# Kernel optimization log

Measured on AMD Instinct MI355X. Metric: run time of the kernel, lower is better.

The kernel has to match this reference:

```python
import jax, jax.numpy as jnp
import numpy as np

N_NODES = 100000


def _gcn_conv(x, W, b, src, dst, num_nodes):
    """PyG-style GCNConv: add self-loops, symmetric normalization, linear.
    x: [N, Fin], W: [Fin, Fout], b: [Fout], src/dst: [E] (already include self-loops).
    """
    h = x @ W  # [N, Fout] transform first (PyG order), keeps edge traffic at Fout width
    ones = jnp.ones(dst.shape[0], dtype=h.dtype)
    deg = jax.ops.segment_sum(ones, dst, num_segments=num_nodes)  # degree of A+I
    dinv = jnp.where(deg > 0, jax.lax.rsqrt(deg), 0.0)
    norm = dinv[src] * dinv[dst]  # [E]
    msg = h[src] * norm[:, None]  # [E, Fout] gather + scale
    out = jax.ops.segment_sum(msg, dst, num_segments=num_nodes)  # scatter-add
    return out + b


def setup_inputs() -> dict:
    key = jax.random.key(0)
    k1, k2, k3, k4, k5 = jax.random.split(key, 5)
    input_dim, hidden_dim, embedding_dim = 128, 64, 32
    x = jax.random.normal(k1, (N_NODES, input_dim), dtype=jnp.float32)
    edge_index = jax.random.randint(k2, (2, 1600000), 0, N_NODES, dtype=jnp.int32)
    # Glorot-like init for weights
    W1 = jax.random.normal(k3, (input_dim, hidden_dim), dtype=jnp.float32) / np.sqrt(input_dim)
    b1 = jnp.zeros((hidden_dim,), dtype=jnp.float32)
    W2 = jax.random.normal(k4, (hidden_dim, embedding_dim), dtype=jnp.float32) / np.sqrt(hidden_dim)
    b2 = jnp.zeros((embedding_dim,), dtype=jnp.float32)
    return {"x": x, "edge_index": edge_index, "W1": W1, "b1": b1, "W2": W2, "b2": b2}


def reference(x, edge_index, W1, b1, W2, b2):
    num_nodes = x.shape[0]
    loop = jnp.arange(num_nodes, dtype=edge_index.dtype)
    src = jnp.concatenate([edge_index[0], loop])  # add self-loops (PyG default)
    dst = jnp.concatenate([edge_index[1], loop])
    h = _gcn_conv(x, W1, b1, src, dst, num_nodes)
    h = jax.nn.relu(h)
    z = _gcn_conv(h, W2, b2, src, dst, num_nodes)
    return z
```

## Files before the change

kernel.cpp:

```cpp
#include <hip/hip_runtime.h>
#include <hip/hip_bf16.h>


#define MAXBUCK 512
#define CURSTRIDE 16

typedef unsigned int uint32;

__device__ __forceinline__ void fma4(float4& a, float s, const float4& w) {
    a.x = fmaf(s, w.x, a.x); a.y = fmaf(s, w.y, a.y);
    a.z = fmaf(s, w.z, a.z); a.w = fmaf(s, w.w, a.w);
}
__device__ __forceinline__ uint32 bf16rn(float f) {
    uint32 u = __float_as_uint(f);
    return (u + 0x7fffu + ((u >> 16) & 1u)) >> 16;
}
__device__ __forceinline__ float bflo(uint32 v) { return __uint_as_float(v << 16); }
__device__ __forceinline__ float bfhi(uint32 v) { return __uint_as_float(v & 0xffff0000u); }

__global__ __launch_bounds__(1024) void k_bin(const int* __restrict__ src,
                                              const int* __restrict__ dst, int E,
                                              int nbuck, int cap,
                                              int* __restrict__ cursor,
                                              uint32* __restrict__ pairs) {
    __shared__ int hist[MAXBUCK];
    __shared__ int base_l[MAXBUCK];
    __shared__ int cur[MAXBUCK];
    __shared__ int dloc[4096];
    int t = threadIdx.x;
    int e0 = blockIdx.x * 4096;
    for (int i = t; i < MAXBUCK; i += 1024) { hist[i] = 0; cur[i] = 0; }
    __syncthreads();
    for (int i = t; i < 4096; i += 1024) {
        int e = e0 + i;
        if (e < E) {
            int d = dst[e];
            dloc[i] = d;
            atomicAdd(&hist[d >> 8], 1);
        }
    }
    __syncthreads();
    for (int i = t; i < nbuck; i += 1024)
        base_l[i] = hist[i] ? (i * cap + atomicAdd(&cursor[i * CURSTRIDE], hist[i])) : 0;
    __syncthreads();
    for (int i = t; i < 4096; i += 1024) {
        int e = e0 + i;
        if (e < E) {
            int d = dloc[i];
            int b = d >> 8;
            int p = atomicAdd(&cur[b], 1);
            int idx = base_l[b] + p;
            if (idx < (b + 1) * cap)
                pairs[idx] = (uint32)src[e] | ((uint32)(d & 255) << 24);
        }
    }
}

__global__ __launch_bounds__(1024) void k_fill2(const uint32* __restrict__ pairs,
                                                const int* __restrict__ bucket_cnt,
                                                int cap, int N,
                                                int* __restrict__ srclist,
                                                int* __restrict__ rowstart,
                                                int* __restrict__ cnt,
                                                float* __restrict__ dinv) {
    __shared__ int hist[256];
    __shared__ int sh[256];
    __shared__ int rs_ex[256];
    __shared__ int cur[256];
    int b = blockIdx.x;
    int t = threadIdx.x;
    int start = b * cap;
    int end = start + min(bucket_cnt[b * CURSTRIDE], cap);
    int node0 = b << 8;

    if (t < 256) { hist[t] = 0; cur[t] = 0; }
    __syncthreads();
    for (int e = start + t; e < end; e += 1024)
        atomicAdd(&hist[pairs[e] >> 24], 1);
    __syncthreads();
    int v = 0;
    if (t < 256) { v = hist[t]; sh[t] = v; }
    __syncthreads();
    for (int off = 1; off < 256; off <<= 1) {
        int tmp = 0;
        if (t < 256 && t >= off) tmp = sh[t - off];
        __syncthreads();
        if (t < 256) sh[t] += tmp;
        __syncthreads();
    }
    if (t < 256) {
        rs_ex[t] = sh[t] - v;
        int node = node0 + t;
        if (node < N) {
            rowstart[node] = start + rs_ex[t];
            cnt[node] = v;
            dinv[node] = rsqrtf((float)(v + 1));
        }
    }
    __syncthreads();
    for (int e = start + t; e < end; e += 1024) {
        uint32 pr = pairs[e];
        int dl = pr >> 24;
        int p = atomicAdd(&cur[dl], 1);
        srclist[start + rs_ex[dl] + p] = (int)(pr & 0x00FFFFFFu);
    }
}

__global__ __launch_bounds__(256) void k_gemm1(const float* __restrict__ x,
                                               const float* __restrict__ W1,
                                               const float* __restrict__ dinv,
                                               uint32* __restrict__ h1b, int n) {
    __shared__ float W1s[64 * 64];
    __shared__ float xs[32][68];
    int t = threadIdx.x;
    int node0 = blockIdx.x * 32;
    int tx = t & 15;
    int ty = t >> 4;
    int na = ty * 2, nb = na + 1;
    float4 acc0 = make_float4(0.f, 0.f, 0.f, 0.f);
    float4 acc1 = make_float4(0.f, 0.f, 0.f, 0.f);
    const float4* W1v = (const float4*)W1;
    const float4* xv = (const float4*)x;
    float4* W1sv = (float4*)W1s;
    const float4* W1sq = (const float4*)W1s;

#pragma unroll 1
    for (int ph = 0; ph < 2; ph++) {
        __syncthreads();
        for (int i = t; i < 1024; i += 256) W1sv[i] = W1v[ph * 1024 + i];
        for (int i = t; i < 512; i += 256) {
            int nl = i >> 4, kq4 = i & 15;
            int node = node0 + nl;
            float4 v = make_float4(0.f, 0.f, 0.f, 0.f);
            if (node < n) v = xv[(size_t)node * 32 + ph * 16 + kq4];
            *(float4*)&xs[nl][kq4 * 4] = v;
        }
        __syncthreads();
#pragma unroll 4
        for (int kq = 0; kq < 16; kq++) {
            float4 xa = *(const float4*)&xs[na][kq * 4];
            float4 xb = *(const float4*)&xs[nb][kq * 4];
            float4 w0 = W1sq[(kq * 4 + 0) * 16 + tx];
            float4 w1 = W1sq[(kq * 4 + 1) * 16 + tx];
            float4 w2 = W1sq[(kq * 4 + 2) * 16 + tx];
            float4 w3 = W1sq[(kq * 4 + 3) * 16 + tx];
            fma4(acc0, xa.x, w0); fma4(acc0, xa.y, w1);
            fma4(acc0, xa.z, w2); fma4(acc0, xa.w, w3);
            fma4(acc1, xb.x, w0); fma4(acc1, xb.y, w1);
            fma4(acc1, xb.z, w2); fma4(acc1, xb.w, w3);
        }
    }
    int nA = node0 + na, nB = node0 + nb;
    if (nA < n) {
        float di = dinv[nA];
        uint2 pk = make_uint2(bf16rn(acc0.x * di) | (bf16rn(acc0.y * di) << 16),
                              bf16rn(acc0.z * di) | (bf16rn(acc0.w * di) << 16));
        ((uint2*)h1b)[(size_t)nA * 16 + tx] = pk;
    }
    if (nB < n) {
        float di = dinv[nB];
        uint2 pk = make_uint2(bf16rn(acc1.x * di) | (bf16rn(acc1.y * di) << 16),
                              bf16rn(acc1.z * di) | (bf16rn(acc1.w * di) << 16));
        ((uint2*)h1b)[(size_t)nB * 16 + tx] = pk;
    }
}

__global__ __launch_bounds__(256) void k_gather_l1(const int* __restrict__ rowstart,
                                                   const int* __restrict__ cnt,
                                                   const int* __restrict__ srclist,
                                                   const uint32* __restrict__ h1b,
                                                   const float* __restrict__ dinv,
                                                   const float* __restrict__ b1,
                                                   const float* __restrict__ W2,
                                                   unsigned short* __restrict__ h2b, int n) {
    __shared__ __align__(16) float W2s[64 * 32];
    __shared__ __align__(16) float hb[8][64];
    int t = threadIdx.x;
    {
        const float4* W2v = (const float4*)W2;
        float4* W2sv = (float4*)W2s;
        W2sv[t] = W2v[t];
        W2sv[t + 256] = W2v[t + 256];
    }
    int wid = t >> 6, lane = t & 63;
    int nodeA = blockIdx.x * 8 + wid * 2;
    int nodeB = nodeA + 1;
    bool validA = (nodeA < n), validB = (nodeB < n);
    int j = lane & 15, q = lane >> 4;

    int rowA = 0, mA = 0, rowB = 0, mB = 0;
    float diA = 0.0f, diB = 0.0f;
    uint2 svA = make_uint2(0u, 0u), svB = make_uint2(0u, 0u);
    const uint2* h1v = (const uint2*)h1b;
    if (validA) { rowA = rowstart[nodeA]; mA = cnt[nodeA]; diA = dinv[nodeA];
                  svA = h1v[(size_t)nodeA * 16 + j]; }
    if (validB) { rowB = rowstart[nodeB]; mB = cnt[nodeB]; diB = dinv[nodeB];
                  svB = h1v[(size_t)nodeB * 16 + j]; }
    int mA0 = min(64, mA), mB0 = min(64, mB);
    int sidxA = (lane < mA0) ? srclist[rowA + lane] : 0;
    int sidxB = (lane < mB0) ? srclist[rowB + lane] : 0;

    float aA0 = 0.f, aA1 = 0.f, aA2 = 0.f, aA3 = 0.f;
    float aB0 = 0.f, aB1 = 0.f, aB2 = 0.f, aB3 = 0.f;
    int jjA = 0, jjB = 0;
    for (; jjA + 16 <= mA0 && jjB + 16 <= mB0; jjA += 16, jjB += 16) {
        int sA0 = __shfl(sidxA, jjA + q),      sA1 = __shfl(sidxA, jjA + 4 + q);
        int sA2 = __shfl(sidxA, jjA + 8 + q),  sA3 = __shfl(sidxA, jjA + 12 + q);
        int sB0 = __shfl(sidxB, jjB + q),      sB1 = __shfl(sidxB, jjB + 4 + q);
        int sB2 = __shfl(sidxB, jjB + 8 + q),  sB3 = __shfl(sidxB, jjB + 12 + q);
        uint2 vA0 = h1v[(size_t)sA0 * 16 + j], vA1 = h1v[(size_t)sA1 * 16 + j];
        uint2 vA2 = h1v[(size_t)sA2 * 16 + j], vA3 = h1v[(size_t)sA3 * 16 + j];
        uint2 vB0 = h1v[(size_t)sB0 * 16 + j], vB1 = h1v[(size_t)sB1 * 16 + j];
        uint2 vB2 = h1v[(size_t)sB2 * 16 + j], vB3 = h1v[(size_t)sB3 * 16 + j];
        aA0 += (bflo(vA0.x) + bflo(vA1.x)) + (bflo(vA2.x) + bflo(vA3.x));
        aA1 += (bfhi(vA0.x) + bfhi(vA1.x)) + (bfhi(vA2.x) + bfhi(vA3.x));
        aA2 += (bflo(vA0.y) + bflo(vA1.y)) + (bflo(vA2.y) + bflo(vA3.y));
        aA3 += (bfhi(vA0.y) + bfhi(vA1.y)) + (bfhi(vA2.y) + bfhi(vA3.y));
        aB0 += (bflo(vB0.x) + bflo(vB1.x)) + (bflo(vB2.x) + bflo(vB3.x));
        aB1 += (bfhi(vB0.x) + bfhi(vB1.x)) + (bfhi(vB2.x) + bfhi(vB3.x));
        aB2 += (bflo(vB0.y) + bflo(vB1.y)) + (bflo(vB2.y) + bflo(vB3.y));
        aB3 += (bfhi(vB0.y) + bfhi(vB1.y)) + (bfhi(vB2.y) + bfhi(vB3.y));
    }
    for (; jjA + 8 <= mA0 && jjB + 8 <= mB0; jjA += 8, jjB += 8) {
        int sA0 = __shfl(sidxA, jjA + q), sA1 = __shfl(sidxA, jjA + 4 + q);
        int sB0 = __shfl(sidxB, jjB + q), sB1 = __shfl(sidxB, jjB + 4 + q);
        uint2 vA0 = h1v[(size_t)sA0 * 16 + j], vA1 = h1v[(size_t)sA1 * 16 + j];
        uint2 vB0 = h1v[(size_t)sB0 * 16 + j], vB1 = h1v[(size_t)sB1 * 16 + j];
        aA0 += bflo(vA0.x) + bflo(vA1.x);
        aA1 += bfhi(vA0.x) + bfhi(vA1.x);
        aA2 += bflo(vA0.y) + bflo(vA1.y);
        aA3 += bfhi(vA0.y) + bfhi(vA1.y);
        aB0 += bflo(vB0.x) + bflo(vB1.x);
        aB1 += bfhi(vB0.x) + bfhi(vB1.x);
        aB2 += bflo(vB0.y) + bflo(vB1.y);
        aB3 += bfhi(vB0.y) + bfhi(vB1.y);
    }
    for (; jjA + 8 <= mA0; jjA += 8) {
        int s0 = __shfl(sidxA, jjA + q), s1 = __shfl(sidxA, jjA + 4 + q);
        uint2 v0 = h1v[(size_t)s0 * 16 + j], v1 = h1v[(size_t)s1 * 16 + j];
        aA0 += bflo(v0.x) + bflo(v1.x);
        aA1 += bfhi(v0.x) + bfhi(v1.x);
        aA2 += bflo(v0.y) + bflo(v1.y);
        aA3 += bfhi(v0.y) + bfhi(v1.y);
    }
    for (; jjA < mA0; jjA += 4) {
        int jidx = jjA + q;
        int s = __shfl(sidxA, min(jidx, mA0 - 1));
        uint2 v = h1v[(size_t)s * 16 + j];
        if (jidx < mA0) {
            aA0 += bflo(v.x); aA1 += bfhi(v.x);
            aA2 += bflo(v.y); aA3 += bfhi(v.y);
        }
    }
    for (; jjB + 8 <= mB0; jjB += 8) {
        int s0 = __shfl(sidxB, jjB + q), s1 = __shfl(sidxB, jjB + 4 + q);
        uint2 v0 = h1v[(size_t)s0 * 16 + j], v1 = h1v[(size_t)s1 * 16 + j];
        aB0 += bflo(v0.x) + bflo(v1.x);
        aB1 += bfhi(v0.x) + bfhi(v1.x);
        aB2 += bflo(v0.y) + bflo(v1.y);
        aB3 += bfhi(v0.y) + bfhi(v1.y);
    }
    for (; jjB < mB0; jjB += 4) {
        int jidx = jjB + q;
        int s = __shfl(sidxB, min(jidx, mB0 - 1));
        uint2 v = h1v[(size_t)s * 16 + j];
        if (jidx < mB0) {
            aB0 += bflo(v.x); aB1 += bfhi(v.x);
            aB2 += bflo(v.y); aB3 += bfhi(v.y);
        }
    }
    for (int j0 = 64; j0 < mA; j0 += 64) {
        int m = min(64, mA - j0);
        int sb = (lane < m) ? srclist[rowA + j0 + lane] : 0;
        int jj = 0;
        for (; jj + 8 <= m; jj += 8) {
            int s0 = __shfl(sb, jj + q), s1 = __shfl(sb, jj + 4 + q);
            uint2 v0 = h1v[(size_t)s0 * 16 + j], v1 = h1v[(size_t)s1 * 16 + j];
            aA0 += bflo(v0.x) + bflo(v1.x);
            aA1 += bfhi(v0.x) + bfhi(v1.x);
            aA2 += bflo(v0.y) + bflo(v1.y);
            aA3 += bfhi(v0.y) + bfhi(v1.y);
        }
        for (; jj < m; jj += 4) {
            int jidx = jj + q;
            int s = __shfl(sb, min(jidx, m - 1));
            uint2 v = h1v[(size_t)s * 16 + j];
            if (jidx < m) {
                aA0 += bflo(v.x); aA1 += bfhi(v.x);
                aA2 += bflo(v.y); aA3 += bfhi(v.y);
            }
        }
    }
    for (int j0 = 64; j0 < mB; j0 += 64) {
        int m = min(64, mB - j0);
        int sb = (lane < m) ? srclist[rowB + j0 + lane] : 0;
        int jj = 0;
        for (; jj + 8 <= m; jj += 8) {
            int s0 = __shfl(sb, jj + q), s1 = __shfl(sb, jj + 4 + q);
            uint2 v0 = h1v[(size_t)s0 * 16 + j], v1 = h1v[(size_t)s1 * 16 + j];
            aB0 += bflo(v0.x) + bflo(v1.x);
            aB1 += bfhi(v0.x) + bfhi(v1.x);
            aB2 += bflo(v0.y) + bflo(v1.y);
            aB3 += bfhi(v0.y) + bfhi(v1.y);
        }
        for (; jj < m; jj += 4) {
            int jidx = jj + q;
            int s = __shfl(sb, min(jidx, m - 1));
            uint2 v = h1v[(size_t)s * 16 + j];
            if (jidx < m) {
                aB0 += bflo(v.x); aB1 += bfhi(v.x);
                aB2 += bflo(v.y); aB3 += bfhi(v.y);
            }
        }
    }

    aA0 += __shfl_xor(aA0, 16); aA0 += __shfl_xor(aA0, 32);
    aA1 += __shfl_xor(aA1, 16); aA1 += __shfl_xor(aA1, 32);
    aA2 += __shfl_xor(aA2, 16); aA2 += __shfl_xor(aA2, 32);
    aA3 += __shfl_xor(aA3, 16); aA3 += __shfl_xor(aA3, 32);
    aB0 += __shfl_xor(aB0, 16); aB0 += __shfl_xor(aB0, 32);
    aB1 += __shfl_xor(aB1, 16); aB1 += __shfl_xor(aB1, 32);
    aB2 += __shfl_xor(aB2, 16); aB2 += __shfl_xor(aB2, 32);
    aB3 += __shfl_xor(aB3, 16); aB3 += __shfl_xor(aB3, 32);
    if (validA && q == 0) {
        float4 bq = ((const float4*)b1)[j];
        float4 hv;
        hv.x = fmaxf((aA0 + bflo(svA.x)) * diA + bq.x, 0.0f);
        hv.y = fmaxf((aA1 + bfhi(svA.x)) * diA + bq.y, 0.0f);
        hv.z = fmaxf((aA2 + bflo(svA.y)) * diA + bq.z, 0.0f);
        hv.w = fmaxf((aA3 + bfhi(svA.y)) * diA + bq.w, 0.0f);
        *(float4*)&hb[wid * 2][4 * j] = hv;
    }
    if (validB && q == 0) {
        float4 bq = ((const float4*)b1)[j];
        float4 hv;
        hv.x = fmaxf((aB0 + bflo(svB.x)) * diB + bq.x, 0.0f);
        hv.y = fmaxf((aB1 + bfhi(svB.x)) * diB + bq.y, 0.0f);
        hv.z = fmaxf((aB2 + bflo(svB.y)) * diB + bq.z, 0.0f);
        hv.w = fmaxf((aB3 + bfhi(svB.y)) * diB + bq.w, 0.0f);
        *(float4*)&hb[wid * 2 + 1][4 * j] = hv;
    }
    __syncthreads();
    int c = lane & 31, half = lane >> 5;
    int k0 = half * 32;
    if (validA) {
        float s = 0.0f;
        const float4* hb4 = (const float4*)&hb[wid * 2][k0];
#pragma unroll
        for (int kk = 0; kk < 8; kk++) {
            float4 h4 = hb4[kk];
            int kb = k0 + kk * 4;
            s = fmaf(h4.x, W2s[(kb + 0) * 32 + c], s);
            s = fmaf(h4.y, W2s[(kb + 1) * 32 + c], s);
            s = fmaf(h4.z, W2s[(kb + 2) * 32 + c], s);
            s = fmaf(h4.w, W2s[(kb + 3) * 32 + c], s);
        }
        s += __shfl_xor(s, 32);
        if (half == 0) h2b[(size_t)nodeA * 32 + c] = (unsigned short)bf16rn(s * diA);
    }
    if (validB) {
        float s = 0.0f;
        const float4* hb4 = (const float4*)&hb[wid * 2 + 1][k0];
#pragma unroll
        for (int kk = 0; kk < 8; kk++) {
            float4 h4 = hb4[kk];
            int kb = k0 + kk * 4;
            s = fmaf(h4.x, W2s[(kb + 0) * 32 + c], s);
            s = fmaf(h4.y, W2s[(kb + 1) * 32 + c], s);
            s = fmaf(h4.z, W2s[(kb + 2) * 32 + c], s);
            s = fmaf(h4.w, W2s[(kb + 3) * 32 + c], s);
        }
        s += __shfl_xor(s, 32);
        if (half == 0) h2b[(size_t)nodeB * 32 + c] = (unsigned short)bf16rn(s * diB);
    }
}

__global__ __launch_bounds__(256) void k_gather_l2(const int* __restrict__ rowstart,
                                                   const int* __restrict__ cnt,
                                                   const int* __restrict__ srclist,
                                                   const uint32* __restrict__ h2b,
                                                   const float* __restrict__ dinv,
                                                   const float* __restrict__ b2v,
                                                   float* __restrict__ out, int n) {
    int t = threadIdx.x;
    int wid = t >> 6, lane = t & 63;
    int nodeA = blockIdx.x * 8 + wid * 2;
    if (nodeA >= n) return;
    int nodeB = nodeA + 1;
    bool validB = (nodeB < n);
    int j = lane & 7, o = lane >> 3;

    int rowA = rowstart[nodeA], mA = cnt[nodeA];
    float diA = dinv[nodeA];
    int rowB = 0, mB = 0;
    float diB = 0.0f;
    const uint2* h2v = (const uint2*)h2b;
    uint2 svA = h2v[(size_t)nodeA * 8 + j];
    uint2 svB = make_uint2(0u, 0u);
    if (validB) { rowB = rowstart[nodeB]; mB = cnt[nodeB]; diB = dinv[nodeB];
                  svB = h2v[(size_t)nodeB * 8 + j]; }
    int mA0 = min(64, mA), mB0 = min(64, mB);
    int sidxA = (lane < mA0) ? srclist[rowA + lane] : 0;
    int sidxB = (lane < mB0) ? srclist[rowB + lane] : 0;

    float aA0 = 0.f, aA1 = 0.f, aA2 = 0.f, aA3 = 0.f;
    float aB0 = 0.f, aB1 = 0.f, aB2 = 0.f, aB3 = 0.f;
    int jjA = 0, jjB = 0;
    for (; jjA + 16 <= mA0 && jjB + 16 <= mB0; jjA += 16, jjB += 16) {
        int sA0 = __shfl(sidxA, jjA + o), sA1 = __shfl(sidxA, jjA + 8 + o);
        int sB0 = __shfl(sidxB, jjB + o), sB1 = __shfl(sidxB, jjB + 8 + o);
        uint2 vA0 = h2v[(size_t)sA0 * 8 + j], vA1 = h2v[(size_t)sA1 * 8 + j];
        uint2 vB0 = h2v[(size_t)sB0 * 8 + j], vB1 = h2v[(size_t)sB1 * 8 + j];
        aA0 += bflo(vA0.x) + bflo(vA1.x);
        aA1 += bfhi(vA0.x) + bfhi(vA1.x);
        aA2 += bflo(vA0.y) + bflo(vA1.y);
        aA3 += bfhi(vA0.y) + bfhi(vA1.y);
        aB0 += bflo(vB0.x) + bflo(vB1.x);
        aB1 += bfhi(vB0.x) + bfhi(vB1.x);
        aB2 += bflo(vB0.y) + bflo(vB1.y);
        aB3 += bfhi(vB0.y) + bfhi(vB1.y);
    }
    for (; jjA + 8 <= mA0 && jjB + 8 <= mB0; jjA += 8, jjB += 8) {
        int sA0 = __shfl(sidxA, jjA + o);
        int sB0 = __shfl(sidxB, jjB + o);
        uint2 vA0 = h2v[(size_t)sA0 * 8 + j];
        uint2 vB0 = h2v[(size_t)sB0 * 8 + j];
        aA0 += bflo(vA0.x); aA1 += bfhi(vA0.x);
        aA2 += bflo(vA0.y); aA3 += bfhi(vA0.y);
        aB0 += bflo(vB0.x); aB1 += bfhi(vB0.x);
        aB2 += bflo(vB0.y); aB3 += bfhi(vB0.y);
    }
    for (; jjA + 8 <= mA0; jjA += 8) {
        int s0 = __shfl(sidxA, jjA + o);
        uint2 v0 = h2v[(size_t)s0 * 8 + j];
        aA0 += bflo(v0.x); aA1 += bfhi(v0.x);
        aA2 += bflo(v0.y); aA3 += bfhi(v0.y);
    }
    if (jjA < mA0) {
        int jidx = jjA + o;
        int s = __shfl(sidxA, min(jidx, mA0 - 1));
        uint2 v = h2v[(size_t)s * 8 + j];
        if (jidx < mA0) {
            aA0 += bflo(v.x); aA1 += bfhi(v.x);
            aA2 += bflo(v.y); aA3 += bfhi(v.y);
        }
    }
    for (; jjB + 8 <= mB0; jjB += 8) {
        int s0 = __shfl(sidxB, jjB + o);
        uint2 v0 = h2v[(size_t)s0 * 8 + j];
        aB0 += bflo(v0.x); aB1 += bfhi(v0.x);
        aB2 += bflo(v0.y); aB3 += bfhi(v0.y);
    }
    if (jjB < mB0) {
        int jidx = jjB + o;
        int s = __shfl(sidxB, min(jidx, mB0 - 1));
        uint2 v = h2v[(size_t)s * 8 + j];
        if (jidx < mB0) {
            aB0 += bflo(v.x); aB1 += bfhi(v.x);
            aB2 += bflo(v.y); aB3 += bfhi(v.y);
        }
    }
    for (int j0 = 64; j0 < mA; j0 += 64) {
        int m = min(64, mA - j0);
        int sb = (lane < m) ? srclist[rowA + j0 + lane] : 0;
        int jj = 0;
        for (; jj + 8 <= m; jj += 8) {
            int s0 = __shfl(sb, jj + o);
            uint2 v0 = h2v[(size_t)s0 * 8 + j];
            aA0 += bflo(v0.x); aA1 += bfhi(v0.x);
            aA2 += bflo(v0.y); aA3 += bfhi(v0.y);
        }
        if (jj < m) {
            int jidx = jj + o;
            int s = __shfl(sb, min(jidx, m - 1));
            uint2 v = h2v[(size_t)s * 8 + j];
            if (jidx < m) {
                aA0 += bflo(v.x); aA1 += bfhi(v.x);
                aA2 += bflo(v.y); aA3 += bfhi(v.y);
            }
        }
    }
    for (int j0 = 64; j0 < mB; j0 += 64) {
        int m = min(64, mB - j0);
        int sb = (lane < m) ? srclist[rowB + j0 + lane] : 0;
        int jj = 0;
        for (; jj + 8 <= m; jj += 8) {
            int s0 = __shfl(sb, jj + o);
            uint2 v0 = h2v[(size_t)s0 * 8 + j];
            aB0 += bflo(v0.x); aB1 += bfhi(v0.x);
            aB2 += bflo(v0.y); aB3 += bfhi(v0.y);
        }
        if (jj < m) {
            int jidx = jj + o;
            int s = __shfl(sb, min(jidx, m - 1));
            uint2 v = h2v[(size_t)s * 8 + j];
            if (jidx < m) {
                aB0 += bflo(v.x); aB1 += bfhi(v.x);
                aB2 += bflo(v.y); aB3 += bfhi(v.y);
            }
        }
    }

    aA0 += __shfl_xor(aA0, 8); aA0 += __shfl_xor(aA0, 16); aA0 += __shfl_xor(aA0, 32);
    aA1 += __shfl_xor(aA1, 8); aA1 += __shfl_xor(aA1, 16); aA1 += __shfl_xor(aA1, 32);
    aA2 += __shfl_xor(aA2, 8); aA2 += __shfl_xor(aA2, 16); aA2 += __shfl_xor(aA2, 32);
    aA3 += __shfl_xor(aA3, 8); aA3 += __shfl_xor(aA3, 16); aA3 += __shfl_xor(aA3, 32);
    aB0 += __shfl_xor(aB0, 8); aB0 += __shfl_xor(aB0, 16); aB0 += __shfl_xor(aB0, 32);
    aB1 += __shfl_xor(aB1, 8); aB1 += __shfl_xor(aB1, 16); aB1 += __shfl_xor(aB1, 32);
    aB2 += __shfl_xor(aB2, 8); aB2 += __shfl_xor(aB2, 16); aB2 += __shfl_xor(aB2, 32);
    aB3 += __shfl_xor(aB3, 8); aB3 += __shfl_xor(aB3, 16); aB3 += __shfl_xor(aB3, 32);
    if (o == 0) {
        float4 bq = ((const float4*)b2v)[j];
        float4 ov;
        ov.x = (aA0 + bflo(svA.x)) * diA + bq.x;
        ov.y = (aA1 + bfhi(svA.x)) * diA + bq.y;
        ov.z = (aA2 + bflo(svA.y)) * diA + bq.z;
        ov.w = (aA3 + bfhi(svA.y)) * diA + bq.w;
        ((float4*)out)[(size_t)nodeA * 8 + j] = ov;
        if (validB) {
            float4 ob;
            ob.x = (aB0 + bflo(svB.x)) * diB + bq.x;
            ob.y = (aB1 + bfhi(svB.x)) * diB + bq.y;
            ob.z = (aB2 + bflo(svB.y)) * diB + bq.z;
            ob.w = (aB3 + bfhi(svB.y)) * diB + bq.w;
            ((float4*)out)[(size_t)nodeB * 8 + j] = ob;
        }
    }
}

extern "C" void kernel_launch(void* const* d_in, const int* in_sizes, int n_in,
                              void* d_out, int out_size, void* d_ws, size_t ws_size,
                              hipStream_t stream) {
    const float* x  = (const float*)d_in[0];
    const int*   ei = (const int*)d_in[1];
    const float* W1 = (const float*)d_in[2];
    const float* b1 = (const float*)d_in[3];
    const float* W2 = (const float*)d_in[4];
    const float* b2 = (const float*)d_in[5];
    float* out = (float*)d_out;

    const int N = in_sizes[0] / 128;
    const int E = in_sizes[1] / 2;
    const int* src = ei;
    const int* dst = ei + E;
    const int nbuck = (N + 255) >> 8;

    int mean = (E + nbuck - 1) / nbuck;
    int cap = (mean + (mean >> 3) + 256 + 63) & ~63;
    size_t region = (size_t)nbuck * cap;

    char* p = (char*)d_ws;
    uint32* pairs      = (uint32*)p;    p += region * 4;
    int* srclist       = (int*)p;       p += region * 4;
    uint32* h1b        = (uint32*)p;    p += (size_t)N * 64 * 2;
    uint32* h2b        = (uint32*)p;    p += (size_t)N * 32 * 2;
    int* cursor        = (int*)p;       p += MAXBUCK * CURSTRIDE * 4;
    int* rowstart      = (int*)p;       p += (size_t)N * 4;
    int* cnt           = (int*)p;       p += (size_t)N * 4;
    float* dinv        = (float*)p;     p += (size_t)N * 4;

    hipMemsetAsync(cursor, 0, (size_t)nbuck * CURSTRIDE * 4, stream);
    k_bin<<<(E + 4095) / 4096, 1024, 0, stream>>>(src, dst, E, nbuck, cap, cursor, pairs);
    k_fill2<<<nbuck, 1024, 0, stream>>>(pairs, cursor, cap, N, srclist, rowstart, cnt, dinv);

    k_gemm1<<<(N + 31) / 32, 256, 0, stream>>>(x, W1, dinv, h1b, N);
    k_gather_l1<<<(N + 7) / 8, 256, 0, stream>>>(rowstart, cnt, srclist, h1b, dinv,
                                                 b1, W2, (unsigned short*)h2b, N);
    k_gather_l2<<<(N + 7) / 8, 256, 0, stream>>>(rowstart, cnt, srclist, h2b, dinv,
                                                 b2, out, N);
}
```

Before: 234.3 us.

## Sort nodes by degree within buckets to balance gather wavefronts

Within each 256-node bucket, k_fill2 now counting-sorts nodes by in-degree (clamped to 63) and writes permuted rowstart, count, dinv and node-id arrays. Both gather kernels walk this permuted slot order, so node pairs that share a wavefront have similar degrees and divergent loop tails shrink. The cost is an extra serial prefix scan in k_fill2, additional permuted metadata arrays, and scattered (non-contiguous) output and self-feature accesses through nid.

```diff
diff --git a/kernel.cpp b/kernel.cpp
--- a/kernel.cpp
+++ b/kernel.cpp
@@ -60,13 +60,17 @@
                                                 const int* __restrict__ bucket_cnt,
                                                 int cap, int N,
                                                 int* __restrict__ srclist,
-                                                int* __restrict__ rowstart,
-                                                int* __restrict__ cnt,
+                                                int* __restrict__ rowstart_p,
+                                                int* __restrict__ cnt_p,
+                                                float* __restrict__ dinv_p,
+                                                int* __restrict__ nid_p,
                                                 float* __restrict__ dinv) {
     __shared__ int hist[256];
     __shared__ int sh[256];
     __shared__ int rs_ex[256];
     __shared__ int cur[256];
+    __shared__ int dh[64];
+    __shared__ int doff[64];
     int b = blockIdx.x;
     int t = threadIdx.x;
     int start = b * cap;
@@ -74,6 +78,7 @@
     int node0 = b << 8;
 
     if (t < 256) { hist[t] = 0; cur[t] = 0; }
+    if (t >= 256 && t < 320) dh[t - 256] = 0;
     __syncthreads();
     for (int e = start + t; e < end; e += 1024)
         atomicAdd(&hist[pairs[e] >> 24], 1);
@@ -88,14 +93,27 @@
         if (t < 256) sh[t] += tmp;
         __syncthreads();
     }
+    int dcl = 0, rank_q = 0;
     if (t < 256) {
         rs_ex[t] = sh[t] - v;
+        dcl = min(v, 63);
+        rank_q = atomicAdd(&dh[dcl], 1);
+    }
+    __syncthreads();
+    if (t == 0) {
+        int acc = 0;
+        for (int i = 0; i < 64; i++) { doff[i] = acc; acc += dh[i]; }
+    }
+    __syncthreads();
+    if (t < 256) {
         int node = node0 + t;
-        if (node < N) {
-            rowstart[node] = start + rs_ex[t];
-            cnt[node] = v;
-            dinv[node] = rsqrtf((float)(v + 1));
-        }
+        int slot = node0 + doff[dcl] + rank_q;
+        nid_p[slot] = node;
+        rowstart_p[slot] = start + rs_ex[t];
+        cnt_p[slot] = (node < N) ? v : 0;
+        float dv = rsqrtf((float)(v + 1));
+        dinv_p[slot] = dv;
+        if (node < N) dinv[node] = dv;
     }
     __syncthreads();
     for (int e = start + t; e < end; e += 1024) {
@@ -165,11 +183,12 @@
     }
 }
 
-__global__ __launch_bounds__(256) void k_gather_l1(const int* __restrict__ rowstart,
-                                                   const int* __restrict__ cnt,
+__global__ __launch_bounds__(256) void k_gather_l1(const int* __restrict__ rowstart_p,
+                                                   const int* __restrict__ cnt_p,
+                                                   const int* __restrict__ nid_p,
+                                                   const float* __restrict__ dinv_p,
                                                    const int* __restrict__ srclist,
                                                    const uint32* __restrict__ h1b,
-                                                   const float* __restrict__ dinv,
                                                    const float* __restrict__ b1,
                                                    const float* __restrict__ W2,
                                                    unsigned short* __restrict__ h2b, int n) {
@@ -183,19 +202,19 @@
         W2sv[t + 256] = W2v[t + 256];
     }
     int wid = t >> 6, lane = t & 63;
-    int nodeA = blockIdx.x * 8 + wid * 2;
-    int nodeB = nodeA + 1;
-    bool validA = (nodeA < n), validB = (nodeB < n);
+    int slotA = blockIdx.x * 8 + wid * 2;
+    int slotB = slotA + 1;
     int j = lane & 15, q = lane >> 4;
 
-    int rowA = 0, mA = 0, rowB = 0, mB = 0;
-    float diA = 0.0f, diB = 0.0f;
+    int nidA = nid_p[slotA], nidB = nid_p[slotB];
+    bool validA = (nidA < n), validB = (nidB < n);
+    int rowA = rowstart_p[slotA], mA = cnt_p[slotA];
+    int rowB = rowstart_p[slotB], mB = cnt_p[slotB];
+    float diA = dinv_p[slotA], diB = dinv_p[slotB];
+    const uint2* h1v = (const uint2*)h1b;
     uint2 svA = make_uint2(0u, 0u), svB = make_uint2(0u, 0u);
-    const uint2* h1v = (const uint2*)h1b;
-    if (validA) { rowA = rowstart[nodeA]; mA = cnt[nodeA]; diA = dinv[nodeA];
-                  svA = h1v[(size_t)nodeA * 16 + j]; }
-    if (validB) { rowB = rowstart[nodeB]; mB = cnt[nodeB]; diB = dinv[nodeB];
-                  svB = h1v[(size_t)nodeB * 16 + j]; }
+    if (validA) svA = h1v[(size_t)nidA * 16 + j];
+    if (validB) svB = h1v[(size_t)nidB * 16 + j];
     int mA0 = min(64, mA), mB0 = min(64, mB);
     int sidxA = (lane < mA0) ? srclist[rowA + lane] : 0;
     int sidxB = (lane < mB0) ? srclist[rowB + lane] : 0;
@@ -356,7 +375,7 @@
             s = fmaf(h4.w, W2s[(kb + 3) * 32 + c], s);
         }
         s += __shfl_xor(s, 32);
-        if (half == 0) h2b[(size_t)nodeA * 32 + c] = (unsigned short)bf16rn(s * diA);
+        if (half == 0) h2b[(size_t)nidA * 32 + c] = (unsigned short)bf16rn(s * diA);
     }
     if (validB) {
         float s = 0.0f;
@@ -371,34 +390,33 @@
             s = fmaf(h4.w, W2s[(kb + 3) * 32 + c], s);
         }
         s += __shfl_xor(s, 32);
-        if (half == 0) h2b[(size_t)nodeB * 32 + c] = (unsigned short)bf16rn(s * diB);
-    }
-}
-
-__global__ __launch_bounds__(256) void k_gather_l2(const int* __restrict__ rowstart,
-                                                   const int* __restrict__ cnt,
+        if (half == 0) h2b[(size_t)nidB * 32 + c] = (unsigned short)bf16rn(s * diB);
+    }
+}
+
+__global__ __launch_bounds__(256) void k_gather_l2(const int* __restrict__ rowstart_p,
+                                                   const int* __restrict__ cnt_p,
+                                                   const int* __restrict__ nid_p,
+                                                   const float* __restrict__ dinv_p,
                                                    const int* __restrict__ srclist,
                                                    const uint32* __restrict__ h2b,
-                                                   const float* __restrict__ dinv,
                                                    const float* __restrict__ b2v,
                                                    float* __restrict__ out, int n) {
     int t = threadIdx.x;
     int wid = t >> 6, lane = t & 63;
-    int nodeA = blockIdx.x * 8 + wid * 2;
-    if (nodeA >= n) return;
-    int nodeB = nodeA + 1;
-    bool validB = (nodeB < n);
+    int slotA = blockIdx.x * 8 + wid * 2;
+    int slotB = slotA + 1;
     int j = lane & 7, o = lane >> 3;
 
-    int rowA = rowstart[nodeA], mA = cnt[nodeA];
-    float diA = dinv[nodeA];
-    int rowB = 0, mB = 0;
-    float diB = 0.0f;
+    int nidA = nid_p[slotA], nidB = nid_p[slotB];
+    bool validA = (nidA < n), validB = (nidB < n);
+    int rowA = rowstart_p[slotA], mA = cnt_p[slotA];
+    int rowB = rowstart_p[slotB], mB = cnt_p[slotB];
+    float diA = dinv_p[slotA], diB = dinv_p[slotB];
     const uint2* h2v = (const uint2*)h2b;
-    uint2 svA = h2v[(size_t)nodeA * 8 + j];
-    uint2 svB = make_uint2(0u, 0u);
-    if (validB) { rowB = rowstart[nodeB]; mB = cnt[nodeB]; diB = dinv[nodeB];
-                  svB = h2v[(size_t)nodeB * 8 + j]; }
+    uint2 svA = make_uint2(0u, 0u), svB = make_uint2(0u, 0u);
+    if (validA) svA = h2v[(size_t)nidA * 8 + j];
+    if (validB) svB = h2v[(size_t)nidB * 8 + j];
     int mA0 = min(64, mA), mB0 = min(64, mB);
     int sidxA = (lane < mA0) ? srclist[rowA + lane] : 0;
     int sidxB = (lane < mB0) ? srclist[rowB + lane] : 0;
@@ -511,19 +529,21 @@
     aB3 += __shfl_xor(aB3, 8); aB3 += __shfl_xor(aB3, 16); aB3 += __shfl_xor(aB3, 32);
     if (o == 0) {
         float4 bq = ((const float4*)b2v)[j];
-        float4 ov;
-        ov.x = (aA0 + bflo(svA.x)) * diA + bq.x;
-        ov.y = (aA1 + bfhi(svA.x)) * diA + bq.y;
-        ov.z = (aA2 + bflo(svA.y)) * diA + bq.z;
-        ov.w = (aA3 + bfhi(svA.y)) * diA + bq.w;
-        ((float4*)out)[(size_t)nodeA * 8 + j] = ov;
+        if (validA) {
+            float4 ov;
+            ov.x = (aA0 + bflo(svA.x)) * diA + bq.x;
+            ov.y = (aA1 + bfhi(svA.x)) * diA + bq.y;
+            ov.z = (aA2 + bflo(svA.y)) * diA + bq.z;
+            ov.w = (aA3 + bfhi(svA.y)) * diA + bq.w;
+            ((float4*)out)[(size_t)nidA * 8 + j] = ov;
+        }
         if (validB) {
             float4 ob;
             ob.x = (aB0 + bflo(svB.x)) * diB + bq.x;
             ob.y = (aB1 + bfhi(svB.x)) * diB + bq.y;
             ob.z = (aB2 + bflo(svB.y)) * diB + bq.z;
             ob.w = (aB3 + bfhi(svB.y)) * diB + bq.w;
-            ((float4*)out)[(size_t)nodeB * 8 + j] = ob;
+            ((float4*)out)[(size_t)nidB * 8 + j] = ob;
         }
     }
 }
@@ -544,6 +564,7 @@
     const int* src = ei;
     const int* dst = ei + E;
     const int nbuck = (N + 255) >> 8;
+    const int nslots = nbuck * 256;
 
     int mean = (E + nbuck - 1) / nbuck;
     int cap = (mean + (mean >> 3) + 256 + 63) & ~63;
@@ -555,17 +576,21 @@
     uint32* h1b        = (uint32*)p;    p += (size_t)N * 64 * 2;
     uint32* h2b        = (uint32*)p;    p += (size_t)N * 32 * 2;
     int* cursor        = (int*)p;       p += MAXBUCK * CURSTRIDE * 4;
-    int* rowstart      = (int*)p;       p += (size_t)N * 4;
-    int* cnt           = (int*)p;       p += (size_t)N * 4;
+    int* rowstart_p    = (int*)p;       p += (size_t)nslots * 4;
+    int* cnt_p         = (int*)p;       p += (size_t)nslots * 4;
+    int* nid_p         = (int*)p;       p += (size_t)nslots * 4;
+    float* dinv_p      = (float*)p;     p += (size_t)nslots * 4;
     float* dinv        = (float*)p;     p += (size_t)N * 4;
 
     hipMemsetAsync(cursor, 0, (size_t)nbuck * CURSTRIDE * 4, stream);
     k_bin<<<(E + 4095) / 4096, 1024, 0, stream>>>(src, dst, E, nbuck, cap, cursor, pairs);
-    k_fill2<<<nbuck, 1024, 0, stream>>>(pairs, cursor, cap, N, srclist, rowstart, cnt, dinv);
+    k_fill2<<<nbuck, 1024, 0, stream>>>(pairs, cursor, cap, N, srclist,
+                                        rowstart_p, cnt_p, dinv_p, nid_p, dinv);
 
     k_gemm1<<<(N + 31) / 32, 256, 0, stream>>>(x, W1, dinv, h1b, N);
-    k_gather_l1<<<(N + 7) / 8, 256, 0, stream>>>(rowstart, cnt, srclist, h1b, dinv,
-                                                 b1, W2, (unsigned short*)h2b, N);
-    k_gather_l2<<<(N + 7) / 8, 256, 0, stream>>>(rowstart, cnt, srclist, h2b, dinv,
-                                                 b2, out, N);
-}
+    k_gather_l1<<<nbuck * 32, 256, 0, stream>>>(rowstart_p, cnt_p, nid_p, dinv_p,
+                                                srclist, h1b, b1, W2,
+                                                (unsigned short*)h2b, N);
+    k_gather_l2<<<nbuck * 32, 256, 0, stream>>>(rowstart_p, cnt_p, nid_p, dinv_p,
+                                                srclist, h2b, b2, out, N);
+}
```

Result: slower. 248.4 us (+6.0%).
